# Kernel tuning notes

Measured on AMD Instinct MI355X. Metric: run time of the kernel, lower is better.

Reference implementation:

```python
import jax, jax.numpy as jnp
import numpy as np

MAX_DEG = 10
DEG_COUNTS = [10000, 130000, 170000, 160000, 100000, 15000, 5000, 2500, 2500, 2500, 2500]
DEG_STARTS = [int(s) for s in np.concatenate([[0], np.cumsum(DEG_COUNTS)[:-1]])]
N_ATOMS = int(sum(DEG_COUNTS))
BATCH = 24000
N_TASKS = 12
IN_FEAT = 75
CHANNELS = [IN_FEAT, 15, 20, 27, 36]


def setup_inputs() -> dict:
    key = jax.random.key(0)
    ks = jax.random.split(key, 32)
    inp = {}
    inp['atom_features'] = jax.random.normal(ks[0], (N_ATOMS, IN_FEAT), dtype=jnp.float32)
    # degree_slice[d] = (start, count) of atoms of degree d (atoms are sorted by degree)
    inp['degree_slice'] = jnp.array(np.stack([DEG_STARTS, DEG_COUNTS], axis=1), dtype=jnp.int32)
    inp['membership'] = jax.random.randint(ks[1], (N_ATOMS,), 0, BATCH, dtype=jnp.int32)
    for d in range(1, MAX_DEG + 1):
        inp[f'deg_adj_{d}'] = jax.random.randint(ks[1 + d], (DEG_COUNTS[d], d), 0, N_ATOMS, dtype=jnp.int32)
    for i in range(4):
        fi, fo = CHANNELS[i], CHANNELS[i + 1]
        inp[f'W{i+1}'] = (jax.random.normal(ks[12 + 2 * i], (2 * MAX_DEG + 1, fi, fo), dtype=jnp.float32)
                          / np.float32(np.sqrt(fi)))
        inp[f'b{i+1}'] = jnp.zeros((2 * MAX_DEG + 1, fo), dtype=jnp.float32)
    inp['W_dense'] = jax.random.normal(ks[30], (2 * CHANNELS[-1], N_TASKS * 2), dtype=jnp.float32) / np.float32(np.sqrt(2 * CHANNELS[-1]))
    inp['b_dense'] = jnp.zeros((N_TASKS * 2,), dtype=jnp.float32)
    return inp


def graph_conv(atoms, deg_adjs, W, b):
    # W: [2*MAX_DEG+1, in, out]; weight iterator order: (rel_d, self_d) for d=1..MAX_DEG, then self_0
    outs = [None] * (MAX_DEG + 1)
    for deg in range(1, MAX_DEG + 1):
        adj = deg_adjs[deg - 1]                      # [n_d, deg] neighbor indices
        rel = jnp.sum(atoms[adj], axis=1)            # gather + sum over neighbors -> [n_d, in]
        s, c = DEG_STARTS[deg], DEG_COUNTS[deg]
        self_atoms = atoms[s:s + c]                  # atoms of this degree (static slice)
        i = 2 * (deg - 1)
        outs[deg] = (rel @ W[i] + b[i]) + (self_atoms @ W[i + 1] + b[i + 1])
    outs[0] = atoms[:DEG_COUNTS[0]] @ W[2 * MAX_DEG] + b[2 * MAX_DEG]
    return jax.nn.selu(jnp.concatenate(outs, axis=0))


def graph_gather(atoms, membership):
    sums = jax.ops.segment_sum(atoms, membership, num_segments=BATCH)
    maxs = jax.ops.segment_max(atoms, membership, num_segments=BATCH)
    return jnp.tanh(jnp.concatenate([sums, maxs], axis=1))  # [BATCH, 2*36]


def reference(atom_features, degree_slice, membership,
              deg_adj_1, deg_adj_2, deg_adj_3, deg_adj_4, deg_adj_5,
              deg_adj_6, deg_adj_7, deg_adj_8, deg_adj_9, deg_adj_10,
              W1, b1, W2, b2, W3, b3, W4, b4, W_dense, b_dense):
    # degree_slice carries the same (start,count) info as the static DEG_STARTS/DEG_COUNTS.
    deg_adjs = [deg_adj_1, deg_adj_2, deg_adj_3, deg_adj_4, deg_adj_5,
                deg_adj_6, deg_adj_7, deg_adj_8, deg_adj_9, deg_adj_10]
    x = graph_conv(atom_features, deg_adjs, W1, b1)
    x = graph_conv(x, deg_adjs, W2, b2)
    x = graph_conv(x, deg_adjs, W3, b3)
    x = graph_conv(x, deg_adjs, W4, b4)
    mol = graph_gather(x, membership)                 # [BATCH, 72]
    logits = (mol @ W_dense + b_dense).reshape(BATCH, N_TASKS, 2)
    return jax.nn.softmax(logits, axis=-1)
```

## Files before the change

kernel.cpp:

```cpp
#include <hip/hip_runtime.h>
#include <hip/hip_fp16.h>
#include <cstdint>

#define NT 256
#define PA 128
#define N_ATOMS_C 600000
#define BATCH_C 24000

constexpr int K_COUNTS[11] = {10000,130000,170000,160000,100000,15000,5000,2500,2500,2500,2500};
constexpr int K_STARTS[11] = {0,10000,140000,310000,470000,570000,585000,590000,592500,595000,597500};
constexpr int DORD[11] = {10,9,8,7,6,5,4,3,2,1,0};

struct AdjPtrs { const int* p[10]; };

typedef _Float16 f16x8 __attribute__((ext_vector_type(8)));
typedef float f32x4 __attribute__((ext_vector_type(4)));

__device__ __forceinline__ float selu_f(float x) {
    const float scale = 1.0507009873554805f;
    const float alpha = 1.6732632423543772f;
    return scale * (x > 0.f ? x : alpha * expm1f(x));
}

__device__ __forceinline__ float2 up2(unsigned u) {
    const __half2 h = __builtin_bit_cast(__half2, u);
    return __half22float2(h);
}
__device__ __forceinline__ unsigned pack2(float a, float b) {
    const __half2 h = __float22half2_rn(make_float2(a, b));
    return __builtin_bit_cast(unsigned, h);
}

template<int NLD4>
__device__ __forceinline__ void load_row(const uint2* __restrict__ p, float* r) {
#pragma unroll
    for (int v = 0; v < NLD4; ++v) {
        const uint2 t = p[v];
        const float2 a = up2(t.x), b = up2(t.y);
        r[4*v] = a.x; r[4*v+1] = a.y; r[4*v+2] = b.x; r[4*v+3] = b.y;
    }
}
template<int NLD4>
__device__ __forceinline__ void add_row(const uint2* __restrict__ p, float* r) {
#pragma unroll
    for (int v = 0; v < NLD4; ++v) {
        const uint2 t = p[v];
        const float2 a = up2(t.x), b = up2(t.y);
        r[4*v] += a.x; r[4*v+1] += a.y; r[4*v+2] += b.x; r[4*v+3] += b.y;
    }
}
template<int NF, int FO>
__device__ __forceinline__ void fma_strip(const float* r, const float* __restrict__ w,
                                          float* acc) {
#pragma unroll
    for (int f = 0; f < NF; ++f)
#pragma unroll
        for (int o = 0; o < FO; ++o)
            acc[o] = fmaf(r[f], w[f * FO + o], acc[o]);
}

template<int TB>
__device__ __forceinline__ void blk2degT(int blk, int& deg, int& s, int& cnt, int& tile) {
    deg = 0; s = 0; cnt = 0; tile = 0;
#pragma unroll
    for (int di = 0; di < 11; ++di) {
        const int d = DORD[di];
        const int nb = (K_COUNTS[d] + TB - 1) / TB;
        if (blk < nb) { deg = d; s = K_STARTS[d]; cnt = K_COUNTS[d]; tile = blk; return; }
        blk -= nb;
    }
}

__global__ __launch_bounds__(256) void prep_kernel(
    const float* __restrict__ x0,
    const float* __restrict__ W,
    const float* __restrict__ bias,
    const int* __restrict__ mem,
    int* __restrict__ cnt,
    unsigned short* __restrict__ z,
    unsigned short* __restrict__ srow)
{
    __shared__ _Float16 sx[PA * 104];

    int deg, s, c, tile;
    blk2degT<PA>(blockIdx.x, deg, s, c, tile);
    const int a0 = tile * PA;
    const int na = min(PA, c - a0);
    const int tid = threadIdx.x;
    const int wi_b = deg ? (2 * deg - 1) : 20;

    const float* src = x0 + (size_t)(s + a0) * 75;
    const int flat = na * 75;
    for (int i4 = tid; i4 * 4 < flat; i4 += NT) {
        const int i = i4 * 4;
        if (i + 4 <= flat) {
            const f32x4 v = *reinterpret_cast<const f32x4*>(src + i);
#pragma unroll
            for (int e = 0; e < 4; ++e) {
                const int j = (i + e) / 75, f = (i + e) - j * 75;
                sx[j * 104 + f] = (_Float16)v[e];
            }
        } else {
            for (int e = 0; i + e < flat; ++e) {
                const int j = (i + e) / 75, f = (i + e) - j * 75;
                sx[j * 104 + f] = (_Float16)src[i + e];
            }
        }
    }
    for (int i = tid; i < PA * 29; i += NT) {
        const int j = i / 29, f = 75 + (i - j * 29);
        sx[j * 104 + f] = (_Float16)0.f;
    }
    __syncthreads();

    if (tid < na) atomicAdd(&cnt[mem[s + a0 + tid]], 1);

    const int lane = tid & 63, w = tid >> 6;
    const int lrow = lane & 15;
    const int kgrp = (lane >> 4) * 8;
    const int row0 = (lane >> 4) * 4;
    const int colo = lane & 15;

    float badd = 0.f;
    if (colo < 15)
        badd = bias[wi_b * 15 + colo] + (deg ? bias[2 * (deg - 1) * 15 + colo] : 0.f);

    f16x8 af[2][3];
#pragma unroll
    for (int mt = 0; mt < 2; ++mt)
#pragma unroll
        for (int ks = 0; ks < 3; ++ks)
            af[mt][ks] = *(const f16x8*)&sx[(w * 32 + mt * 16 + lrow) * 104 + ks * 32 + kgrp];

#pragma unroll
    for (int nt = 0; nt < 5; ++nt) {
        const int wi = (nt < 4) ? 2 * nt : wi_b;
        const float* Wp = W + wi * 1125;
        f16x8 bf[3];
#pragma unroll
        for (int ks = 0; ks < 3; ++ks) {
#pragma unroll
            for (int j = 0; j < 8; ++j) {
                const int k = ks * 32 + kgrp + j;
                float v = 0.f;
                if (k < 75 && lrow < 15) v = Wp[k * 15 + lrow];
                bf[ks][j] = (_Float16)v;
            }
        }
#pragma unroll
        for (int mt = 0; mt < 2; ++mt) {
            f32x4 acc = {0.f, 0.f, 0.f, 0.f};
#pragma unroll
            for (int ks = 0; ks < 3; ++ks)
                acc = __builtin_amdgcn_mfma_f32_16x16x32_f16(af[mt][ks], bf[ks], acc, 0, 0, 0);
#pragma unroll
            for (int reg = 0; reg < 4; ++reg) {
                const int ar = w * 32 + mt * 16 + row0 + reg;
                if (ar < na) {
                    const size_t atom = (size_t)(s + a0 + ar);
                    if (nt < 4) {
                        z[(size_t)nt * ((size_t)N_ATOMS_C * 16) + atom * 16 + colo] =
                            __builtin_bit_cast(unsigned short, (_Float16)acc[reg]);
                    } else {
                        const float v = (colo < 15) ? acc[reg] + badd : 0.f;
                        srow[atom * 16 + colo] =
                            __builtin_bit_cast(unsigned short, (_Float16)v);
                    }
                }
            }
        }
    }
}

__global__ __launch_bounds__(256) void conv1_kernel(
    const float* __restrict__ x0,
    const unsigned short* __restrict__ z,
    const unsigned short* __restrict__ srow,
    const float* __restrict__ W,
    AdjPtrs adjp,
    unsigned short* __restrict__ y1)
{
    int deg, s, c, tile;
    blk2degT<NT>(blockIdx.x, deg, s, c, tile);
    const int a = tile * NT + threadIdx.x;
    if (a >= c) return;
    const int atom = s + a;

    float acc[15];
    {
        const uint2* sp = reinterpret_cast<const uint2*>(srow + (size_t)atom * 16);
        float r[16];
        load_row<4>(sp, r);
#pragma unroll
        for (int o = 0; o < 15; ++o) acc[o] = r[o];
    }

    if (deg >= 1 && deg <= 4) {
        const unsigned short* zd = z + (size_t)(deg - 1) * ((size_t)N_ATOMS_C * 16);
        const int* ad = adjp.p[deg - 1] + (size_t)a * deg;
        int nb[4];
#pragma unroll
        for (int k = 0; k < 4; ++k) nb[k] = ad[k < deg ? k : 0];
        uint4 t[4][2];
#pragma unroll
        for (int k = 0; k < 4; ++k) {
            const uint4* p = reinterpret_cast<const uint4*>(zd + (size_t)nb[k] * 16);
            t[k][0] = p[0]; t[k][1] = p[1];
        }
#pragma unroll
        for (int k = 0; k < 4; ++k) {
            if (k < deg) {
                const unsigned w[8] = {t[k][0].x, t[k][0].y, t[k][0].z, t[k][0].w,
                                       t[k][1].x, t[k][1].y, t[k][1].z, t[k][1].w};
#pragma unroll
                for (int v = 0; v < 8; ++v) {
                    const float2 lo = up2(w[v]);
                    if (2 * v < 15)     acc[2 * v]     += lo.x;
                    if (2 * v + 1 < 15) acc[2 * v + 1] += lo.y;
                }
            }
        }
    } else if (deg >= 5) {
        const float* Wa = W + 2 * (deg - 1) * 1125;
        const int* ad = adjp.p[deg - 1] + (size_t)a * deg;
#pragma unroll 1
        for (int st = 0; st < 3; ++st) {
            float r[25];
#pragma unroll
            for (int j = 0; j < 25; ++j) r[j] = 0.f;
            for (int k = 0; k < deg; ++k) {
                const float* xr = x0 + (size_t)ad[k] * 75 + st * 25;
#pragma unroll
                for (int j = 0; j < 25; ++j) r[j] += xr[j];
            }
            fma_strip<25, 15>(r, Wa + st * 25 * 15, acc);
        }
    }

    uint2* yp = reinterpret_cast<uint2*>(y1 + (size_t)atom * 16);
    float o_[16];
#pragma unroll
    for (int o = 0; o < 16; ++o) o_[o] = (o < 15) ? selu_f(acc[o]) : 0.f;
    yp[0] = make_uint2(pack2(o_[0],o_[1]),  pack2(o_[2],o_[3]));
    yp[1] = make_uint2(pack2(o_[4],o_[5]),  pack2(o_[6],o_[7]));
    yp[2] = make_uint2(pack2(o_[8],o_[9]),  pack2(o_[10],o_[11]));
    yp[3] = make_uint2(pack2(o_[12],o_[13]),pack2(o_[14],o_[15]));
}

template<int FIN, int FINP, int FO, int FOP, int FS>
__global__ __launch_bounds__(256) void conv_kernel(
    const unsigned short* __restrict__ x,
    const float* __restrict__ W,
    const float* __restrict__ bias,
    AdjPtrs adjp,
    unsigned short* __restrict__ y)
{
    static_assert(FS % 4 == 0 && FINP % 4 == 0 && FOP % 4 == 0, "");
    constexpr int NSF = FIN / FS;
    constexpr int TF  = FIN - NSF * FS;
    constexpr int TLD4 = (TF + 3) / 4;
    static_assert(NSF * FS + TLD4 * 4 <= FINP, "tail reads past row");

    int deg, s, c, tile;
    blk2degT<NT>(blockIdx.x, deg, s, c, tile);
    const int a = tile * NT + threadIdx.x;
    if (a >= c) return;
    const int atom = s + a;

    const int wi_a = (deg == 0) ? 20 : 2 * (deg - 1);
    const int wi_b = (deg == 0) ? 20 : 2 * deg - 1;
    const float* Wa = W + wi_a * FIN * FO;
    const float* Wb = W + wi_b * FIN * FO;

    float acc[FO];
#pragma unroll
    for (int o = 0; o < FO; ++o)
        acc[o] = bias[wi_b * FO + o] + ((deg > 0) ? bias[wi_a * FO + o] : 0.f);

    const int* myadj = (deg > 0) ? (adjp.p[deg - 1] + (size_t)a * deg) : nullptr;
    const uint2* selfrow = reinterpret_cast<const uint2*>(x + (size_t)atom * FINP);

#pragma unroll 1
    for (int st = 0; st < NSF; ++st) {
        const int f0 = st * FS;
        float r[FS];
        load_row<FS / 4>(selfrow + (f0 >> 2), r);
        fma_strip<FS, FO>(r, Wb + f0 * FO, acc);
        if (deg > 0) {
#pragma unroll
            for (int f = 0; f < FS; ++f) r[f] = 0.f;
            for (int k = 0; k < deg; ++k)
                add_row<FS / 4>(reinterpret_cast<const uint2*>(
                    x + (size_t)myadj[k] * FINP) + (f0 >> 2), r);
            fma_strip<FS, FO>(r, Wa + f0 * FO, acc);
        }
    }
    if constexpr (TF > 0) {
        constexpr int f0 = NSF * FS;
        float r[TLD4 * 4];
        load_row<TLD4>(selfrow + (f0 >> 2), r);
        fma_strip<TF, FO>(r, Wb + f0 * FO, acc);
        if (deg > 0) {
#pragma unroll
            for (int f = 0; f < TLD4 * 4; ++f) r[f] = 0.f;
            for (int k = 0; k < deg; ++k)
                add_row<TLD4>(reinterpret_cast<const uint2*>(
                    x + (size_t)myadj[k] * FINP) + (f0 >> 2), r);
            fma_strip<TF, FO>(r, Wa + f0 * FO, acc);
        }
    }

    float outv[FOP];
#pragma unroll
    for (int o = 0; o < FOP; ++o) outv[o] = (o < FO) ? selu_f(acc[o]) : 0.f;
    uint2* yp = reinterpret_cast<uint2*>(y + (size_t)atom * FOP);
#pragma unroll
    for (int v = 0; v < FOP / 4; ++v)
        yp[v] = make_uint2(pack2(outv[4*v], outv[4*v+1]),
                           pack2(outv[4*v+2], outv[4*v+3]));
}

__global__ __launch_bounds__(256) void zero_cnt_kernel(int* __restrict__ cnt) {
    const int i = blockIdx.x * NT + threadIdx.x;
    if (i < BATCH_C) cnt[i] = 0;
}
__global__ __launch_bounds__(1024) void scan_kernel(const int* __restrict__ cnt,
                                                    int* __restrict__ base,
                                                    int* __restrict__ cursor) {
    __shared__ int part[1024];
    const int tid = threadIdx.x;
    constexpr int CH = 24;
    const int i0 = tid * CH;
    int sum = 0;
    for (int j = 0; j < CH; ++j) { const int i = i0 + j; if (i < BATCH_C) sum += cnt[i]; }
    part[tid] = sum;
    __syncthreads();
    for (int off = 1; off < 1024; off <<= 1) {
        const int v = (tid >= off) ? part[tid - off] : 0;
        __syncthreads(); part[tid] += v; __syncthreads();
    }
    int run = part[tid] - sum;
    for (int j = 0; j < CH; ++j) {
        const int i = i0 + j;
        if (i < BATCH_C) { base[i] = run; cursor[i] = run; run += cnt[i]; }
    }
    if (tid == 1023) base[BATCH_C] = part[1023];
}
__global__ __launch_bounds__(256) void scatter_kernel(const int* __restrict__ mem,
                                                      int* __restrict__ cursor,
                                                      int* __restrict__ alist) {
    const int i = blockIdx.x * NT + threadIdx.x;
    if (i < N_ATOMS_C) { const int p = atomicAdd(&cursor[mem[i]], 1); alist[p] = i; }
}

__global__ __launch_bounds__(256) void reduce_dense_kernel(
    const unsigned short* __restrict__ y4,
    const int* __restrict__ base, const int* __restrict__ alist,
    const float* __restrict__ Wd, const float* __restrict__ bd,
    float* __restrict__ out)
{
    __shared__ float sW[72 * 24];
    __shared__ float sb[24];
    __shared__ float molf[4][72];

    const int tid = threadIdx.x;
    for (int i = tid; i < 72 * 24; i += NT) sW[i] = Wd[i];
    if (tid < 24) sb[tid] = bd[tid];
    __syncthreads();

    const int w = tid >> 6, lane = tid & 63;
    const int mol = blockIdx.x * 4 + w;
    const int b0 = base[mol], b1 = base[mol + 1];

    if (lane < 36) {
        float s = 0.f, mx = -INFINITY;
        for (int k = b0; k < b1; ++k) {
            const int atom = alist[k];
            const float v = __half2float(__builtin_bit_cast(__half,
                                y4[(size_t)atom * 36 + lane]));
            s += v; mx = fmaxf(mx, v);
        }
        molf[w][lane] = tanhf(s);
        molf[w][36 + lane] = tanhf(mx);
    }
    __syncthreads();

    if (lane < 24) {
        float l = sb[lane];
#pragma unroll
        for (int f = 0; f < 72; ++f) l += molf[w][f] * sW[f * 24 + lane];
        const float lp = __shfl_xor(l, 1);
        const float m2 = fmaxf(l, lp);
        const float e = expf(l - m2), ep = expf(lp - m2);
        out[(size_t)mol * 24 + lane] = e / (e + ep);
    }
}

extern "C" void kernel_launch(void* const* d_in, const int* in_sizes, int n_in,
                              void* d_out, int out_size, void* d_ws, size_t ws_size,
                              hipStream_t stream)
{
    const float* x0         = (const float*)d_in[0];
    const int*   membership = (const int*)d_in[2];
    AdjPtrs adj;
    for (int d = 0; d < 10; ++d) adj.p[d] = (const int*)d_in[3 + d];
    const float *W1=(const float*)d_in[13], *b1=(const float*)d_in[14];
    const float *W2=(const float*)d_in[15], *b2=(const float*)d_in[16];
    const float *W3=(const float*)d_in[17], *b3=(const float*)d_in[18];
    const float *W4=(const float*)d_in[19], *b4=(const float*)d_in[20];
    const float *Wd=(const float*)d_in[21], *bd=(const float*)d_in[22];

    const size_t szA = 81600000;
    const size_t szB = 38400000;
    const size_t nInts = (size_t)N_ATOMS_C + (BATCH_C + 1) + BATCH_C + BATCH_C;
    if (ws_size < szA + szB + nInts * 4) return;

    char* base0 = (char*)d_ws;
    unsigned short* zbuf = (unsigned short*)base0;
    unsigned short* y2   = (unsigned short*)base0;
    unsigned short* y4   = (unsigned short*)(base0 + 38400000);
    unsigned short* srow = (unsigned short*)(base0 + szA);
    unsigned short* y1   = (unsigned short*)(base0 + szA + 19200000);
    unsigned short* y3   = (unsigned short*)(base0 + szA);
    int* alist  = (int*)(base0 + szA + szB);
    int* base   = alist + N_ATOMS_C;
    int* cursor = base + (BATCH_C + 1);
    int* cnt    = cursor + BATCH_C;

    int nblk = 0, nblkp = 0;
    for (int d = 0; d < 11; ++d) {
        nblk  += (K_COUNTS[d] + NT - 1) / NT;
        nblkp += (K_COUNTS[d] + PA - 1) / PA;
    }
    const int nb_atoms = (N_ATOMS_C + NT - 1) / NT;

    zero_cnt_kernel<<<(BATCH_C + NT - 1) / NT, NT, 0, stream>>>(cnt);
    prep_kernel<<<nblkp, NT, 0, stream>>>(x0, W1, b1, membership, cnt, zbuf, srow);
    scan_kernel<<<1, 1024, 0, stream>>>(cnt, base, cursor);
    scatter_kernel<<<nb_atoms, NT, 0, stream>>>(membership, cursor, alist);

    conv1_kernel<<<nblk, NT, 0, stream>>>(x0, zbuf, srow, W1, adj, y1);
    conv_kernel<15,16,20,32,16><<<nblk, NT, 0, stream>>>(y1, W2, b2, adj, y2);
    conv_kernel<20,32,27,32,32><<<nblk, NT, 0, stream>>>(y2, W3, b3, adj, y3);
    conv_kernel<27,32,36,36,32><<<nblk, NT, 0, stream>>>(y3, W4, b4, adj, y4);

    reduce_dense_kernel<<<BATCH_C / 4, NT, 0, stream>>>(y4, base, alist, Wd, bd, (float*)d_out);
}
```

Baseline: 629.1 us.

## Prepack fp16 weight tiles and stage prep outputs through LDS for wide stores

```diff
diff --git a/kernel.cpp b/kernel.cpp
--- a/kernel.cpp
+++ b/kernel.cpp
@@ -6,6 +6,8 @@
 #define PA 128
 #define N_ATOMS_C 600000
 #define BATCH_C 24000
+#define BT_STRIDE 104
+#define SO_STRIDE 88
 
 constexpr int K_COUNTS[11] = {10000,130000,170000,160000,100000,15000,5000,2500,2500,2500,2500};
 constexpr int K_STARTS[11] = {0,10000,140000,310000,470000,570000,585000,590000,592500,595000,597500};
@@ -71,9 +73,23 @@
     }
 }
 
+__global__ __launch_bounds__(256) void bprep_kernel(const float* __restrict__ W,
+                                                    unsigned short* __restrict__ Bt)
+{
+    const int idx = blockIdx.x * NT + threadIdx.x;
+    if (idx >= 11 * 80 * BT_STRIDE) return;
+    const int deg = idx / (80 * BT_STRIDE);
+    const int rem = idx - deg * (80 * BT_STRIDE);
+    const int col = rem / BT_STRIDE, k = rem - col * BT_STRIDE;
+    const int p = col >> 4, o = col & 15;
+    const int wi = (p < 4) ? 2 * p : (deg ? 2 * deg - 1 : 20);
+    const float v = (k < 75 && o < 15) ? W[wi * 1125 + k * 15 + o] : 0.f;
+    Bt[idx] = __builtin_bit_cast(unsigned short, (_Float16)v);
+}
+
 __global__ __launch_bounds__(256) void prep_kernel(
     const float* __restrict__ x0,
-    const float* __restrict__ W,
+    const unsigned short* __restrict__ Bt,
     const float* __restrict__ bias,
     const int* __restrict__ mem,
     int* __restrict__ cnt,
@@ -81,6 +97,7 @@
     unsigned short* __restrict__ srow)
 {
     __shared__ _Float16 sx[PA * 104];
+    __shared__ _Float16 sb[80 * BT_STRIDE];
 
     int deg, s, c, tile;
     blk2degT<PA>(blockIdx.x, deg, s, c, tile);
@@ -93,23 +110,21 @@
     const int flat = na * 75;
     for (int i4 = tid; i4 * 4 < flat; i4 += NT) {
         const int i = i4 * 4;
-        if (i + 4 <= flat) {
-            const f32x4 v = *reinterpret_cast<const f32x4*>(src + i);
-#pragma unroll
-            for (int e = 0; e < 4; ++e) {
-                const int j = (i + e) / 75, f = (i + e) - j * 75;
-                sx[j * 104 + f] = (_Float16)v[e];
-            }
-        } else {
-            for (int e = 0; i + e < flat; ++e) {
-                const int j = (i + e) / 75, f = (i + e) - j * 75;
-                sx[j * 104 + f] = (_Float16)src[i + e];
-            }
+        const f32x4 v = *reinterpret_cast<const f32x4*>(src + i);
+#pragma unroll
+        for (int e = 0; e < 4; ++e) {
+            const int j = (i + e) / 75, f = (i + e) - j * 75;
+            sx[j * 104 + f] = (_Float16)v[e];
         }
     }
     for (int i = tid; i < PA * 29; i += NT) {
         const int j = i / 29, f = 75 + (i - j * 29);
         sx[j * 104 + f] = (_Float16)0.f;
+    }
+    {
+        const uint4* bsrc = reinterpret_cast<const uint4*>(Bt + (size_t)deg * 80 * BT_STRIDE);
+        uint4* bdst = reinterpret_cast<uint4*>(sb);
+        for (int i = tid; i < 80 * BT_STRIDE / 8; i += NT) bdst[i] = bsrc[i];
     }
     __syncthreads();
 
@@ -131,22 +146,16 @@
 #pragma unroll
         for (int ks = 0; ks < 3; ++ks)
             af[mt][ks] = *(const f16x8*)&sx[(w * 32 + mt * 16 + lrow) * 104 + ks * 32 + kgrp];
+    __syncthreads();
+
+    _Float16* sout = sx;
 
 #pragma unroll
     for (int nt = 0; nt < 5; ++nt) {
-        const int wi = (nt < 4) ? 2 * nt : wi_b;
-        const float* Wp = W + wi * 1125;
         f16x8 bf[3];
 #pragma unroll
-        for (int ks = 0; ks < 3; ++ks) {
-#pragma unroll
-            for (int j = 0; j < 8; ++j) {
-                const int k = ks * 32 + kgrp + j;
-                float v = 0.f;
-                if (k < 75 && lrow < 15) v = Wp[k * 15 + lrow];
-                bf[ks][j] = (_Float16)v;
-            }
-        }
+        for (int ks = 0; ks < 3; ++ks)
+            bf[ks] = *(const f16x8*)&sb[(nt * 16 + lrow) * BT_STRIDE + ks * 32 + kgrp];
 #pragma unroll
         for (int mt = 0; mt < 2; ++mt) {
             f32x4 acc = {0.f, 0.f, 0.f, 0.f};
@@ -156,19 +165,25 @@
 #pragma unroll
             for (int reg = 0; reg < 4; ++reg) {
                 const int ar = w * 32 + mt * 16 + row0 + reg;
-                if (ar < na) {
-                    const size_t atom = (size_t)(s + a0 + ar);
-                    if (nt < 4) {
-                        z[(size_t)nt * ((size_t)N_ATOMS_C * 16) + atom * 16 + colo] =
-                            __builtin_bit_cast(unsigned short, (_Float16)acc[reg]);
-                    } else {
-                        const float v = (colo < 15) ? acc[reg] + badd : 0.f;
-                        srow[atom * 16 + colo] =
-                            __builtin_bit_cast(unsigned short, (_Float16)v);
-                    }
-                }
+                float v = acc[reg];
+                if (nt == 4) v = (colo < 15) ? v + badd : 0.f;
+                sout[ar * SO_STRIDE + nt * 16 + colo] = (_Float16)v;
             }
         }
+    }
+    __syncthreads();
+
+    const int nunits = na * 5;
+    for (int u = tid; u < nunits; u += NT) {
+        const int al = u / 5, p = u - al * 5;
+        const uint4* sp = reinterpret_cast<const uint4*>(&sout[al * SO_STRIDE + p * 16]);
+        const uint4 v0 = sp[0], v1 = sp[1];
+        const size_t atom = (size_t)(s + a0 + al);
+        unsigned short* dst = (p < 4)
+            ? (z + (size_t)p * ((size_t)N_ATOMS_C * 16) + atom * 16)
+            : (srow + atom * 16);
+        uint4* dq = reinterpret_cast<uint4*>(dst);
+        dq[0] = v0; dq[1] = v1;
     }
 }
 
@@ -413,7 +428,8 @@
     const size_t szA = 81600000;
     const size_t szB = 38400000;
     const size_t nInts = (size_t)N_ATOMS_C + (BATCH_C + 1) + BATCH_C + BATCH_C;
-    if (ws_size < szA + szB + nInts * 4) return;
+    const size_t btOff = szA + szB + nInts * 4;
+    if (ws_size < btOff + (size_t)11 * 80 * BT_STRIDE * 2) return;
 
     char* base0 = (char*)d_ws;
     unsigned short* zbuf = (unsigned short*)base0;
@@ -426,6 +442,7 @@
     int* base   = alist + N_ATOMS_C;
     int* cursor = base + (BATCH_C + 1);
     int* cnt    = cursor + BATCH_C;
+    unsigned short* Bt = (unsigned short*)(base0 + btOff);
 
     int nblk = 0, nblkp = 0;
     for (int d = 0; d < 11; ++d) {
@@ -435,7 +452,8 @@
     const int nb_atoms = (N_ATOMS_C + NT - 1) / NT;
 
     zero_cnt_kernel<<<(BATCH_C + NT - 1) / NT, NT, 0, stream>>>(cnt);
-    prep_kernel<<<nblkp, NT, 0, stream>>>(x0, W1, b1, membership, cnt, zbuf, srow);
+    bprep_kernel<<<(11 * 80 * BT_STRIDE + NT - 1) / NT, NT, 0, stream>>>(W1, Bt);
+    prep_kernel<<<nblkp, NT, 0, stream>>>(x0, Bt, b1, membership, cnt, zbuf, srow);
     scan_kernel<<<1, 1024, 0, stream>>>(cnt, base, cursor);
     scatter_kernel<<<nb_atoms, NT, 0, stream>>>(membership, cursor, alist);
 
```

Result: faster. 526.1 us (-16.4%).
